# Performance work log

Hardware: AMD Instinct MI355X
Metric: run time of the kernel (lower is better)

The kernel has to match this reference:

```python
import jax, jax.numpy as jnp
import numpy as np

T, R, H, DK = 2, 3, 4, 32
IN_DIM, OUT_DIM = 128, 128
N = 50000
E = 400000
RELS = [(0, 1), (1, 0), (1, 1)]  # (src_type, dst_type) per relation


def setup_inputs() -> dict:
    key = jax.random.key(0)
    ks = jax.random.split(key, 24)
    lin_scale = float(np.sqrt(2.0 / (IN_DIM + OUT_DIM)))
    att_scale = float(np.sqrt(2.0 / (DK + DK)))
    inp = {
        'h0': jax.random.normal(ks[0], (N, IN_DIM), jnp.float32),
        'h1': jax.random.normal(ks[1], (N, IN_DIM), jnp.float32),
        'Wk': jax.random.normal(ks[2], (T, IN_DIM, OUT_DIM), jnp.float32) * lin_scale,
        'bk': jnp.zeros((T, OUT_DIM), jnp.float32),
        'Wq': jax.random.normal(ks[3], (T, IN_DIM, OUT_DIM), jnp.float32) * lin_scale,
        'bq': jnp.zeros((T, OUT_DIM), jnp.float32),
        'Wv': jax.random.normal(ks[4], (T, IN_DIM, OUT_DIM), jnp.float32) * lin_scale,
        'bv': jnp.zeros((T, OUT_DIM), jnp.float32),
        'Wa': jax.random.normal(ks[5], (T, OUT_DIM, OUT_DIM), jnp.float32) * lin_scale,
        'ba': jnp.zeros((T, OUT_DIM), jnp.float32),
        'rel_att': jax.random.normal(ks[6], (R, H, DK, DK), jnp.float32) * att_scale,
        'rel_msg': jax.random.normal(ks[7], (R, H, DK, DK), jnp.float32) * att_scale,
        'rel_pri': jnp.ones((R, H), jnp.float32),
        'skip': jnp.ones((T,), jnp.float32),
        'src0': jax.random.randint(ks[8], (E,), 0, N, jnp.int32),
        'dst0': jax.random.randint(ks[9], (E,), 0, N, jnp.int32),
        'src1': jax.random.randint(ks[10], (E,), 0, N, jnp.int32),
        'dst1': jax.random.randint(ks[11], (E,), 0, N, jnp.int32),
        'src2': jax.random.randint(ks[12], (E,), 0, N, jnp.int32),
        'dst2': jax.random.randint(ks[13], (E,), 0, N, jnp.int32),
    }
    return inp


def _hgt_forward(h0, h1, Wk, bk, Wq, bq, Wv, bv, Wa, ba,
                 rel_att, rel_msg, rel_pri, skip, edges):
    sqrt_dk = np.sqrt(DK).astype(np.float32)
    hs = [h0, h1]
    # per-type k/q/v projections, reshaped to [N, H, DK]
    k_all = [(hs[t] @ Wk[t] + bk[t]).reshape(-1, H, DK) for t in range(T)]
    q_all = [(hs[t] @ Wq[t] + bq[t]).reshape(-1, H, DK) for t in range(T)]
    v_all = [(hs[t] @ Wv[t] + bv[t]).reshape(-1, H, DK) for t in range(T)]
    agg = {0: [], 1: []}
    for r, (s, d) in enumerate(RELS):
        src, dst = edges[r]
        k = jnp.einsum('nhi,hij->nhj', k_all[s], rel_att[r])
        v = jnp.einsum('nhi,hij->nhj', v_all[s], rel_msg[r])
        q = q_all[d]
        # edge-wise dot-product attention score [E, H]
        score = jnp.einsum('ehd,ehd->eh', q[dst], k[src]) * rel_pri[r] / sqrt_dk
        # edge softmax normalized by destination node
        m = jax.ops.segment_max(score, dst, num_segments=N)
        e = jnp.exp(score - m[dst])
        z = jax.ops.segment_sum(e, dst, num_segments=N)
        a = e / z[dst]
        msg = v[src] * a[..., None]  # [E, H, DK]
        agg[d].append(jax.ops.segment_sum(msg, dst, num_segments=N))
    outs = []
    for t in range(T):
        tmean = agg[t][0]
        for extra in agg[t][1:]:
            tmean = tmean + extra
        tmean = tmean / jnp.float32(len(agg[t]))  # cross_reducer='mean'
        tt = tmean.reshape(-1, OUT_DIM)
        trans = tt @ Wa[t] + ba[t]  # dropout p=0 -> identity
        alpha = jax.nn.sigmoid(skip[t])
        outs.append(trans * alpha + hs[t] * (1.0 - alpha))
    return jnp.stack(outs)  # [T, N, OUT_DIM]


def reference(h0, h1, Wk, bk, Wq, bq, Wv, bv, Wa, ba,
              rel_att, rel_msg, rel_pri, skip,
              src0, dst0, src1, dst1, src2, dst2):
    edges = [(src0, dst0), (src1, dst1), (src2, dst2)]
    return _hgt_forward(h0, h1, Wk, bk, Wq, bq, Wv, bv, Wa, ba,
                        rel_att, rel_msg, rel_pri, skip, edges)
```

## Files before the change

kernel.cpp:

```cpp
#include <hip/hip_runtime.h>
#include <hip/hip_bf16.h>
#include <math.h>


#define NN 50000
#define EE 400000
#define CAP 40

typedef __bf16 bf16x8 __attribute__((ext_vector_type(8)));
typedef float floatx4 __attribute__((ext_vector_type(4)));
typedef _Float16 h2 __attribute__((ext_vector_type(2)));

#if __has_builtin(__builtin_amdgcn_exp2f)
#define EXP2F(x) __builtin_amdgcn_exp2f(x)
#else
#define EXP2F(x) exp2f(x)
#endif

__device__ __forceinline__ h2 u_to_h2(unsigned int u) {
    union { unsigned int u; h2 h; } x; x.u = u; return x.h;
}

__device__ __forceinline__ float dot2f(h2 a, h2 b, float c) {
#if __has_builtin(__builtin_amdgcn_fdot2)
    return __builtin_amdgcn_fdot2(a, b, c, false);
#else
    return fmaf((float)a.x, (float)b.x, fmaf((float)a.y, (float)b.y, c));
#endif
}

__device__ __forceinline__ float xor1_add(float x) {
#if __has_builtin(__builtin_amdgcn_mov_dpp)
    int y = __builtin_amdgcn_mov_dpp(__float_as_int(x), 0xB1, 0xf, 0xf, true);
    return x + __int_as_float(y);
#else
    return x + __shfl_xor(x, 1);
#endif
}
__device__ __forceinline__ float xor2_add(float x) {
#if __has_builtin(__builtin_amdgcn_mov_dpp)
    int y = __builtin_amdgcn_mov_dpp(__float_as_int(x), 0x4E, 0xf, 0xf, true);
    return x + __int_as_float(y);
#else
    return x + __shfl_xor(x, 2);
#endif
}
__device__ __forceinline__ float xor4_add(float x) {
#if __has_builtin(__builtin_amdgcn_ds_swizzle)
    int y = __builtin_amdgcn_ds_swizzle(__float_as_int(x), 0x101F);
    return x + __int_as_float(y);
#else
    return x + __shfl_xor(x, 4);
#endif
}

#define FUSEB 640
__global__ __launch_bounds__(256) void prep(
    const float* __restrict__ Wk, const float* __restrict__ bk,
    const float* __restrict__ Wq, const float* __restrict__ bq,
    const float* __restrict__ Wv, const float* __restrict__ bv,
    const float* __restrict__ rel_att, const float* __restrict__ rel_msg,
    const float* __restrict__ rel_pri, const float* __restrict__ Wa,
    __hip_bfloat16* __restrict__ Wcat0T, __hip_bfloat16* __restrict__ Wcat1T,
    __hip_bfloat16* __restrict__ WaT,
    float* __restrict__ bcat0, float* __restrict__ bcat1)
{
    int idx = blockIdx.x * 256 + threadIdx.x;
    const int R1 = 128 * 384, R2 = 128 * 640, R3 = 2 * 128 * 128;
    if (idx >= R1 + R2 + R3) return;
    if (idx >= R1 + R2) {
        int t = idx - R1 - R2;
        int tt = t >> 14, rem = t & 16383;
        int k = rem >> 7, col = rem & 127;
        WaT[tt * 16384 + col * 128 + k] = __float2bfloat16(Wa[tt * 16384 + k * 128 + col]);
        return;
    }
    int typ, i, col;
    __hip_bfloat16* Wout; float* bout;
    if (idx < R1) { typ = 0; i = idx / 384; col = idx % 384; Wout = Wcat0T; bout = bcat0; }
    else { idx -= R1; typ = 1; i = idx / 640; col = idx % 640; Wout = Wcat1T; bout = bcat1; }
    float w, b;
    if (col < 128) {
        w = Wq[(typ * 128 + i) * 128 + col];
        b = bq[typ * 128 + col];
    } else {
        int kvcol = col - 128;
        int r = (typ == 0) ? 0 : (1 + (kvcol >> 8));
        int gc = kvcol & 255;
        int isV = (gc >> 2) & 1;
        int c = (gc >> 3) * 4 + (gc & 3);
        int s = typ;
        const float* Wsrc = isV ? Wv : Wk;
        const float* bsrc = isV ? bv : bk;
        const float* rel  = isV ? rel_msg : rel_att;
        int h = c >> 5, j = c & 31;
        float acc = 0.f, bacc = 0.f;
        #pragma unroll
        for (int cc = 0; cc < 32; ++cc) {
            float rr = rel[((r * 4 + h) * 32 + cc) * 32 + j];
            acc  += Wsrc[(s * 128 + i) * 128 + h * 32 + cc] * rr;
            bacc += bsrc[s * 128 + h * 32 + cc] * rr;
        }
        if (!isV) {
            float sc = rel_pri[r * 4 + h] * (0.17677669529663687f * 1.4426950408889634f);
            acc *= sc; bacc *= sc;
        }
        w = acc; b = bacc;
    }
    Wout[col * 128 + i] = __float2bfloat16(w);
    if (i == 0) bout[col] = b;
}

#define SCATB 196
#define SCATX 294
__global__ __launch_bounds__(256) void proj_both(
    const float* __restrict__ h0, const float* __restrict__ h1,
    const __hip_bfloat16* __restrict__ W0T, const __hip_bfloat16* __restrict__ W1T,
    const float* __restrict__ b0, const float* __restrict__ b1,
    ushort* __restrict__ Q0, ushort* __restrict__ Q1,
    ushort* __restrict__ KV0, ushort* __restrict__ KV1,
    ushort* __restrict__ KV2,
    const int* __restrict__ s0, const int* __restrict__ d0,
    const int* __restrict__ s1, const int* __restrict__ d1,
    const int* __restrict__ s2, const int* __restrict__ d2,
    int* __restrict__ cursor, int* __restrict__ sorted_src)
{
    __shared__ __align__(16) __hip_bfloat16 As[128][136];
    __shared__ __align__(16) ushort Bs[128][136];
    const int tid = threadIdx.x;

    if (blockIdx.x < SCATX) {
        int sb = blockIdx.y * SCATX + blockIdx.x;
        int r = sb / SCATB;
        int blk = sb - r * SCATB;
        const int* S = (r == 0) ? s0 : (r == 1) ? s1 : s2;
        const int* D = (r == 0) ? d0 : (r == 1) ? d1 : d2;
        int e0 = blk * 2048 + tid * 8;
        if (e0 + 8 <= EE) {
            int sv[8], dv[8], pos[8];
            *(int4*)&sv[0] = *(const int4*)(S + e0);
            *(int4*)&sv[4] = *(const int4*)(S + e0 + 4);
            *(int4*)&dv[0] = *(const int4*)(D + e0);
            *(int4*)&dv[4] = *(const int4*)(D + e0 + 4);
            #pragma unroll
            for (int j = 0; j < 8; ++j)
                pos[j] = atomicAdd(&cursor[r * NN + dv[j]], 1);
            #pragma unroll
            for (int j = 0; j < 8; ++j)
                if (pos[j] < CAP)
                    sorted_src[(size_t)(r * NN + dv[j]) * CAP + pos[j]] = sv[j];
        } else {
            for (int j = 0; j < 8; ++j) {
                int e = e0 + j;
                if (e >= EE) break;
                int idx = r * NN + D[e];
                int pos = atomicAdd(&cursor[idx], 1);
                if (pos < CAP) sorted_src[(size_t)idx * CAP + pos] = S[e];
            }
        }
        return;
    }

    const int row0 = (blockIdx.x - SCATX) * 128;
    const int typ = blockIdx.y;
    const float* A = typ ? h1 : h0;
    const __hip_bfloat16* WT = typ ? W1T : W0T;
    const float* bias = typ ? b1 : b0;
    const int ntiles = typ ? 5 : 3;

    #pragma unroll
    for (int it = 0; it < 16; ++it) {
        int li = it * 256 + tid;
        int r = li >> 5, k4 = (li & 31) * 4;
        int grow = row0 + r;
        float4 a4 = make_float4(0.f, 0.f, 0.f, 0.f);
        if (grow < NN) a4 = *(const float4*)(A + (size_t)grow * 128 + k4);
        As[r][k4 + 0] = __float2bfloat16(a4.x);
        As[r][k4 + 1] = __float2bfloat16(a4.y);
        As[r][k4 + 2] = __float2bfloat16(a4.z);
        As[r][k4 + 3] = __float2bfloat16(a4.w);
    }

    const int lane = tid & 63;
    const int wv = tid >> 6;
    const int wr = (wv & 1) * 64, wc = (wv >> 1) * 64;
    const int lr = lane & 15, kq = lane >> 4;

    for (int ct = 0; ct < ntiles; ++ct) {
        __syncthreads();
        #pragma unroll
        for (int it = 0; it < 8; ++it) {
            int li = it * 256 + tid;
            int c = li >> 4, k8 = (li & 15) * 8;
            *(uint4*)&Bs[c][k8] = *(const uint4*)(WT + (size_t)(ct * 128 + c) * 128 + k8);
        }
        __syncthreads();

        floatx4 acc[4][4];
        #pragma unroll
        for (int i = 0; i < 4; ++i)
            #pragma unroll
            for (int j = 0; j < 4; ++j)
                acc[i][j] = (floatx4){0.f, 0.f, 0.f, 0.f};

        #pragma unroll
        for (int kc = 0; kc < 128; kc += 32) {
            bf16x8 a[4], b[4];
            #pragma unroll
            for (int i = 0; i < 4; ++i) a[i] = *(const bf16x8*)&As[wr + i * 16 + lr][kc + kq * 8];
            #pragma unroll
            for (int j = 0; j < 4; ++j) b[j] = *(const bf16x8*)&Bs[wc + j * 16 + lr][kc + kq * 8];
            #pragma unroll
            for (int i = 0; i < 4; ++i)
                #pragma unroll
                for (int j = 0; j < 4; ++j)
                    acc[i][j] = __builtin_amdgcn_mfma_f32_16x16x32_bf16(a[i], b[j], acc[i][j], 0, 0, 0);
        }

        float biasv[4];
        #pragma unroll
        for (int j = 0; j < 4; ++j) biasv[j] = bias[ct * 128 + wc + j * 16 + lr];

        __syncthreads();
        #pragma unroll
        for (int i = 0; i < 4; ++i)
            #pragma unroll
            for (int reg = 0; reg < 4; ++reg) {
                int row = wr + i * 16 + kq * 4 + reg;
                #pragma unroll
                for (int j = 0; j < 4; ++j) {
                    union { _Float16 h; ushort s; } cv;
                    cv.h = (_Float16)(acc[i][j][reg] + biasv[j]);
                    Bs[row][wc + j * 16 + lr] = cv.s;
                }
            }
        __syncthreads();

        ushort* plane; int ld, toff;
        if (ct == 0) { plane = typ ? Q1 : Q0; ld = 128; toff = 0; }
        else {
            int rel = typ ? (1 + ((ct - 1) >> 1)) : 0;
            plane = (rel == 0) ? KV0 : (rel == 1) ? KV1 : KV2;
            ld = 256; toff = ((ct - 1) & 1) * 128;
        }
        #pragma unroll
        for (int it = 0; it < 8; ++it) {
            int li = it * 256 + tid;
            int row = li >> 4, chunk = (li & 15) * 8;
            int grow = row0 + row;
            if (grow < NN)
                *(uint4*)(plane + (size_t)grow * ld + toff + chunk) = *(const uint4*)&Bs[row][chunk];
        }
    }
}

__device__ __forceinline__ void epi_body(
    char* smem,
    const __hip_bfloat16* __restrict__ A0, const __hip_bfloat16* __restrict__ A1, float ascale,
    const __hip_bfloat16* __restrict__ BT, const float* __restrict__ bias,
    float* __restrict__ C, const float* __restrict__ skipGate, const float* __restrict__ Hres)
{
    typedef __hip_bfloat16 bfrow[136];
    bfrow* As = (bfrow*)smem;
    bfrow* Bs = (bfrow*)(smem + 128 * 136 * 2);
    typedef float frow[132];
    frow* St = (frow*)smem;
    const int tid = threadIdx.x;
    const int row0 = blockIdx.x * 128;

    #pragma unroll
    for (int it = 0; it < 8; ++it) {
        int li = it * 256 + tid;
        int c = li >> 4, k8 = (li & 15) * 8;
        *(uint4*)&Bs[c][k8] = *(const uint4*)(BT + (size_t)c * 128 + k8);
    }
    #pragma unroll
    for (int it = 0; it < 8; ++it) {
        int li = it * 256 + tid;
        int r = li >> 4, k8 = (li & 15) * 8;
        int grow = row0 + r;
        __hip_bfloat162 o2[4];
        if (grow < NN) {
            const __hip_bfloat162* pa = (const __hip_bfloat162*)(A0 + (size_t)grow * 128 + k8);
            if (A1) {
                const __hip_bfloat162* pb = (const __hip_bfloat162*)(A1 + (size_t)grow * 128 + k8);
                #pragma unroll
                for (int u = 0; u < 4; ++u) {
                    float2 fa = __bfloat1622float2(pa[u]);
                    float2 fb = __bfloat1622float2(pb[u]);
                    fa.x = (fa.x + fb.x) * ascale;
                    fa.y = (fa.y + fb.y) * ascale;
                    o2[u] = __float22bfloat162_rn(fa);
                }
            } else {
                #pragma unroll
                for (int u = 0; u < 4; ++u) o2[u] = pa[u];
            }
        } else {
            __hip_bfloat162 zz = __float22bfloat162_rn(make_float2(0.f, 0.f));
            #pragma unroll
            for (int u = 0; u < 4; ++u) o2[u] = zz;
        }
        __hip_bfloat162* dst = (__hip_bfloat162*)&As[r][k8];
        #pragma unroll
        for (int u = 0; u < 4; ++u) dst[u] = o2[u];
    }
    __syncthreads();

    const int lane = tid & 63;
    const int wv = tid >> 6;
    const int wr = (wv & 1) * 64, wc = (wv >> 1) * 64;
    const int lr = lane & 15, kq = lane >> 4;

    floatx4 acc[4][4];
    #pragma unroll
    for (int i = 0; i < 4; ++i)
        #pragma unroll
        for (int j = 0; j < 4; ++j)
            acc[i][j] = (floatx4){0.f, 0.f, 0.f, 0.f};

    #pragma unroll
    for (int kc = 0; kc < 128; kc += 32) {
        bf16x8 a[4], b[4];
        #pragma unroll
        for (int i = 0; i < 4; ++i) a[i] = *(const bf16x8*)&As[wr + i * 16 + lr][kc + kq * 8];
        #pragma unroll
        for (int j = 0; j < 4; ++j) b[j] = *(const bf16x8*)&Bs[wc + j * 16 + lr][kc + kq * 8];
        #pragma unroll
        for (int i = 0; i < 4; ++i)
            #pragma unroll
            for (int j = 0; j < 4; ++j)
                acc[i][j] = __builtin_amdgcn_mfma_f32_16x16x32_bf16(a[i], b[j], acc[i][j], 0, 0, 0);
    }

    float sg = *skipGate;
    float alpha = 1.f / (1.f + expf(-sg));
    float beta = 1.f - alpha;
    float biasv[4];
    #pragma unroll
    for (int j = 0; j < 4; ++j) biasv[j] = bias[wc + j * 16 + lr];

    __syncthreads();
    #pragma unroll
    for (int i = 0; i < 4; ++i)
        #pragma unroll
        for (int reg = 0; reg < 4; ++reg) {
            int row = wr + i * 16 + kq * 4 + reg;
            #pragma unroll
            for (int j = 0; j < 4; ++j)
                St[row][wc + j * 16 + lr] = acc[i][j][reg] + biasv[j];
        }
    __syncthreads();

    #pragma unroll
    for (int it = 0; it < 16; ++it) {
        int li = it * 256 + tid;
        int row = li >> 5, chunk = (li & 31) * 4;
        int grow = row0 + row;
        if (grow < NN) {
            float4 v = *(const float4*)&St[row][chunk];
            float4 hr = *(const float4*)(Hres + (size_t)grow * 128 + chunk);
            v.x = v.x * alpha + hr.x * beta;
            v.y = v.y * alpha + hr.y * beta;
            v.z = v.z * alpha + hr.z * beta;
            v.w = v.w * alpha + hr.w * beta;
            *(float4*)(C + (size_t)grow * 128 + chunk) = v;
        }
    }
}

__global__ __launch_bounds__(256) void epi_both(
    const __hip_bfloat16* __restrict__ aggR0, const __hip_bfloat16* __restrict__ aggR1,
    const __hip_bfloat16* __restrict__ aggR2,
    const __hip_bfloat16* __restrict__ WaT, const float* __restrict__ ba,
    float* __restrict__ out, const float* __restrict__ skip,
    const float* __restrict__ h0, const float* __restrict__ h1)
{
    __shared__ __align__(16) char smem[128 * 136 * 2 * 2];
    if (blockIdx.y == 0)
        epi_body(smem, aggR1, nullptr, 1.f, WaT, ba, out, skip, h0);
    else
        epi_body(smem, aggR0, aggR2, 0.5f, WaT + 16384, ba + 128,
                 out + (size_t)NN * 128, skip + 1, h1);
}

__device__ __forceinline__ void edge4_accum(
    uint4 ra, uint4 rb, uint4 rc, uint4 rd,
    bool mA, bool mB, bool mC, bool mD,
    h2 q01, h2 q23,
    float& z, float& u0, float& u1, float& u2, float& u3)
{
    float pa = dot2f(u_to_h2(ra.x), q01, 0.f); pa = dot2f(u_to_h2(ra.y), q23, pa);
    float pb = dot2f(u_to_h2(rb.x), q01, 0.f); pb = dot2f(u_to_h2(rb.y), q23, pb);
    float pc = dot2f(u_to_h2(rc.x), q01, 0.f); pc = dot2f(u_to_h2(rc.y), q23, pc);
    float pd = dot2f(u_to_h2(rd.x), q01, 0.f); pd = dot2f(u_to_h2(rd.y), q23, pd);
    pa = xor1_add(pa); pb = xor1_add(pb); pc = xor1_add(pc); pd = xor1_add(pd);
    pa = xor2_add(pa); pb = xor2_add(pb); pc = xor2_add(pc); pd = xor2_add(pd);
    pa = xor4_add(pa); pb = xor4_add(pb); pc = xor4_add(pc); pd = xor4_add(pd);
    float ea = EXP2F(pa); if (!mA) ea = 0.f;
    float eb = EXP2F(pb); if (!mB) eb = 0.f;
    float ec = EXP2F(pc); if (!mC) ec = 0.f;
    float ed = EXP2F(pd); if (!mD) ed = 0.f;
    z += (ea + eb) + (ec + ed);
    h2 va, vb;
    va = u_to_h2(ra.z); vb = u_to_h2(ra.w);
    u0 = fmaf(ea, (float)va.x, u0); u1 = fmaf(ea, (float)va.y, u1);
    u2 = fmaf(ea, (float)vb.x, u2); u3 = fmaf(ea, (float)vb.y, u3);
    va = u_to_h2(rb.z); vb = u_to_h2(rb.w);
    u0 = fmaf(eb, (float)va.x, u0); u1 = fmaf(eb, (float)va.y, u1);
    u2 = fmaf(eb, (float)vb.x, u2); u3 = fmaf(eb, (float)vb.y, u3);
    va = u_to_h2(rc.z); vb = u_to_h2(rc.w);
    u0 = fmaf(ec, (float)va.x, u0); u1 = fmaf(ec, (float)va.y, u1);
    u2 = fmaf(ec, (float)vb.x, u2); u3 = fmaf(ec, (float)vb.y, u3);
    va = u_to_h2(rd.z); vb = u_to_h2(rd.w);
    u0 = fmaf(ed, (float)va.x, u0); u1 = fmaf(ed, (float)va.y, u1);
    u2 = fmaf(ed, (float)vb.x, u2); u3 = fmaf(ed, (float)vb.y, u3);
}

__global__ __launch_bounds__(256) void aggregate_all(
    const ushort* __restrict__ Q0, const ushort* __restrict__ Q1,
    const ushort* __restrict__ KV0, const ushort* __restrict__ KV1,
    const ushort* __restrict__ KV2,
    const int* __restrict__ sorted, const int* __restrict__ counts,
    __hip_bfloat16* __restrict__ aggR0, __hip_bfloat16* __restrict__ aggR1,
    __hip_bfloat16* __restrict__ aggR2)
{
    int n = (blockIdx.x * 256 + threadIdx.x) >> 6;
    int lane = threadIdx.x & 63;
    int r = blockIdx.y;
    const ushort *Q, *KV; __hip_bfloat16* outp;
    if (r == 0)      { Q = Q1; KV = KV0; outp = aggR0; }
    else if (r == 1) { Q = Q0; KV = KV1; outp = aggR1; }
    else             { Q = Q1; KV = KV2; outp = aggR2; }
    int gw = r * NN + n;

    int hl = lane & 31;
    int half = lane >> 5;

    int cnt = min(counts[gw], CAP);
    uint2 qr = *(const uint2*)(Q + (size_t)n * 128 + hl * 4);
    const int* elist = sorted + (size_t)gw * CAP;
    int4 v0 = *(const int4*)elist;
    int4 v1 = *(const int4*)(elist + 4);
    int4 v2 = *(const int4*)(elist + 8);
    int4 v3 = *(const int4*)(elist + 12);

    int i0 = half ? v0.y : v0.x;
    int i1 = half ? v0.w : v0.z;
    int i2 = half ? v1.y : v1.x;
    int i3 = half ? v1.w : v1.z;
    int j0 = half ? v2.y : v2.x;
    int j1 = half ? v2.w : v2.z;
    int j2 = half ? v3.y : v3.x;
    int j3 = half ? v3.w : v3.z;
    uint4 ra = *(const uint4*)(KV + (size_t)(unsigned)(i0 * 256 + hl * 8));
    uint4 rb = *(const uint4*)(KV + (size_t)(unsigned)(i1 * 256 + hl * 8));
    uint4 rc = *(const uint4*)(KV + (size_t)(unsigned)(i2 * 256 + hl * 8));
    uint4 rd = *(const uint4*)(KV + (size_t)(unsigned)(i3 * 256 + hl * 8));
    uint4 sa = *(const uint4*)(KV + (size_t)(unsigned)(j0 * 256 + hl * 8));
    uint4 sb = *(const uint4*)(KV + (size_t)(unsigned)(j1 * 256 + hl * 8));
    uint4 sc = *(const uint4*)(KV + (size_t)(unsigned)(j2 * 256 + hl * 8));
    uint4 sd = *(const uint4*)(KV + (size_t)(unsigned)(j3 * 256 + hl * 8));

    h2 q01 = u_to_h2(qr.x), q23 = u_to_h2(qr.y);

    bool mA = (0 + half) < cnt, mB = (2 + half) < cnt, mC = (4 + half) < cnt, mD = (6 + half) < cnt;
    float u0 = 0.f, u1 = 0.f, u2 = 0.f, u3 = 0.f, z = 0.f;
    edge4_accum(ra, rb, rc, rd, mA, mB, mC, mD, q01, q23, z, u0, u1, u2, u3);

    if (cnt > 8) {
        bool nA = (8 + half) < cnt, nB = (10 + half) < cnt, nC = (12 + half) < cnt, nD = (14 + half) < cnt;
        edge4_accum(sa, sb, sc, sd, nA, nB, nC, nD, q01, q23, z, u0, u1, u2, u3);

        for (int i = 16; i < cnt; i += 4) {
            int eA = i + half, eB = i + 2 + half;
            int sA = elist[min(eA, cnt - 1)];
            int sB = elist[min(eB, cnt - 1)];
            uint4 ta = *(const uint4*)(KV + (size_t)(unsigned)(sA * 256 + hl * 8));
            uint4 tb = *(const uint4*)(KV + (size_t)(unsigned)(sB * 256 + hl * 8));
            float pa = dot2f(u_to_h2(ta.x), q01, 0.f); pa = dot2f(u_to_h2(ta.y), q23, pa);
            float pb = dot2f(u_to_h2(tb.x), q01, 0.f); pb = dot2f(u_to_h2(tb.y), q23, pb);
            pa = xor1_add(pa); pb = xor1_add(pb);
            pa = xor2_add(pa); pb = xor2_add(pb);
            pa = xor4_add(pa); pb = xor4_add(pb);
            float ea = EXP2F(pa);
            float eb = EXP2F(pb);
            if (eA >= cnt) ea = 0.f;
            if (eB >= cnt) eb = 0.f;
            z += ea + eb;
            h2 va = u_to_h2(ta.z), vb = u_to_h2(ta.w);
            u0 = fmaf(ea, (float)va.x, u0); u1 = fmaf(ea, (float)va.y, u1);
            u2 = fmaf(ea, (float)vb.x, u2); u3 = fmaf(ea, (float)vb.y, u3);
            va = u_to_h2(tb.z); vb = u_to_h2(tb.w);
            u0 = fmaf(eb, (float)va.x, u0); u1 = fmaf(eb, (float)va.y, u1);
            u2 = fmaf(eb, (float)vb.x, u2); u3 = fmaf(eb, (float)vb.y, u3);
        }
    }

    z  += __shfl_xor(z, 32);
    u0 += __shfl_xor(u0, 32);
    u1 += __shfl_xor(u1, 32);
    u2 += __shfl_xor(u2, 32);
    u3 += __shfl_xor(u3, 32);
    if (half == 0) {
        float inv = (cnt > 0) ? 1.f / z : 0.f;
        __hip_bfloat162 o0 = __float22bfloat162_rn(make_float2(u0 * inv, u1 * inv));
        __hip_bfloat162 o1 = __float22bfloat162_rn(make_float2(u2 * inv, u3 * inv));
        union { uint2 u; __hip_bfloat162 h[2]; } pk2;
        pk2.h[0] = o0; pk2.h[1] = o1;
        *(uint2*)(outp + (size_t)n * 128 + hl * 4) = pk2.u;
    }
}

extern "C" void kernel_launch(void* const* d_in, const int* in_sizes, int n_in,
                              void* d_out, int out_size, void* d_ws, size_t ws_size,
                              hipStream_t stream)
{
    const float* h0      = (const float*)d_in[0];
    const float* h1      = (const float*)d_in[1];
    const float* Wk      = (const float*)d_in[2];
    const float* bk      = (const float*)d_in[3];
    const float* Wq      = (const float*)d_in[4];
    const float* bq      = (const float*)d_in[5];
    const float* Wv      = (const float*)d_in[6];
    const float* bv      = (const float*)d_in[7];
    const float* Wa      = (const float*)d_in[8];
    const float* ba      = (const float*)d_in[9];
    const float* rel_att = (const float*)d_in[10];
    const float* rel_msg = (const float*)d_in[11];
    const float* rel_pri = (const float*)d_in[12];
    const float* skip    = (const float*)d_in[13];
    const int*   src0    = (const int*)d_in[14];
    const int*   dst0    = (const int*)d_in[15];
    const int*   src1    = (const int*)d_in[16];
    const int*   dst1    = (const int*)d_in[17];
    const int*   src2    = (const int*)d_in[18];
    const int*   dst2    = (const int*)d_in[19];
    float* out = (float*)d_out;

    char* w = (char*)d_ws;
    auto alloc = [&](size_t bytes) -> char* {
        char* p = w; w += (bytes + 255) & ~(size_t)255; return p;
    };
    __hip_bfloat16* Wcat0T = (__hip_bfloat16*)alloc(384 * 128 * 2);
    __hip_bfloat16* Wcat1T = (__hip_bfloat16*)alloc(640 * 128 * 2);
    __hip_bfloat16* WaT    = (__hip_bfloat16*)alloc(2 * 128 * 128 * 2);
    float* bcat0 = (float*)alloc(384 * sizeof(float));
    float* bcat1 = (float*)alloc(640 * sizeof(float));
    ushort* Q0  = (ushort*)alloc((size_t)NN * 128 * 2);
    ushort* Q1  = (ushort*)alloc((size_t)NN * 128 * 2);
    ushort* KV0 = (ushort*)alloc((size_t)NN * 256 * 2);
    ushort* KV1 = (ushort*)alloc((size_t)NN * 256 * 2);
    ushort* KV2 = (ushort*)alloc((size_t)NN * 256 * 2);
    __hip_bfloat16* aggR0 = (__hip_bfloat16*)alloc((size_t)NN * 128 * 2);
    __hip_bfloat16* aggR1 = (__hip_bfloat16*)alloc((size_t)NN * 128 * 2);
    __hip_bfloat16* aggR2 = (__hip_bfloat16*)alloc((size_t)NN * 128 * 2);
    int* cursor  = (int*)alloc(3 * NN * sizeof(int));
    int* sorted  = (int*)alloc((size_t)3 * NN * CAP * sizeof(int));

    if ((size_t)(w - (char*)d_ws) > ws_size) return;

    size_t zlen = (size_t)((char*)sorted - (char*)cursor) + (size_t)3 * NN * CAP * sizeof(int);
    hipMemsetAsync(cursor, 0, zlen, stream);

    prep<<<FUSEB, 256, 0, stream>>>(
        Wk, bk, Wq, bq, Wv, bv, rel_att, rel_msg, rel_pri, Wa,
        Wcat0T, Wcat1T, WaT, bcat0, bcat1);

    const int ROWB = (NN + 127) / 128;
    proj_both<<<dim3(SCATX + ROWB, 2), 256, 0, stream>>>(
        h0, h1, Wcat0T, Wcat1T, bcat0, bcat1,
        Q0, Q1, KV0, KV1, KV2,
        src0, dst0, src1, dst1, src2, dst2, cursor, sorted);

    const int AG = (NN * 64) / 256;
    aggregate_all<<<dim3(AG, 3), 256, 0, stream>>>(Q0, Q1, KV0, KV1, KV2, sorted, cursor,
                                                   aggR0, aggR1, aggR2);

    epi_both<<<dim3(ROWB, 2), 256, 0, stream>>>(aggR0, aggR1, aggR2, WaT, ba, out, skip, h0, h1);
}
```

Measured before the change: 349.8 us.

## Replace global-atomic CSR build with two-pass shared-memory bucket sort

Edge bucketing by destination now runs as a two-pass bucket sort. The prep kernel partitions each edge block into 256-node destination buckets using shared-memory atomics, packing the source index and the low destination bits into one int. proj_both then gathers each bucket's slices, builds per-row lists in shared memory and writes them out coalesced, which removes the global atomics and the large workspace memset. It also defers the second group of KV loads in aggregation until cnt>8 and reuses the aggR0 buffer as scratch. The risks are silent truncation if a bucket slice overflows SLICE=40 and the 16-bit source packing, which only works because N fits in 16 bits.

```diff
diff --git a/kernel.cpp b/kernel.cpp
--- a/kernel.cpp
+++ b/kernel.cpp
@@ -6,6 +6,8 @@
 #define NN 50000
 #define EE 400000
 #define CAP 40
+#define NBKT 196
+#define SLICE 40
 
 typedef __bf16 bf16x8 __attribute__((ext_vector_type(8)));
 typedef float floatx4 __attribute__((ext_vector_type(4)));
@@ -63,8 +65,53 @@
     const float* __restrict__ rel_pri, const float* __restrict__ Wa,
     __hip_bfloat16* __restrict__ Wcat0T, __hip_bfloat16* __restrict__ Wcat1T,
     __hip_bfloat16* __restrict__ WaT,
-    float* __restrict__ bcat0, float* __restrict__ bcat1)
+    float* __restrict__ bcat0, float* __restrict__ bcat1,
+    const int* __restrict__ s0, const int* __restrict__ d0,
+    const int* __restrict__ s1, const int* __restrict__ d1,
+    const int* __restrict__ s2, const int* __restrict__ d2,
+    int* __restrict__ seg, int* __restrict__ cnt2)
 {
+    __shared__ int cur[NBKT];
+    if (blockIdx.x >= FUSEB) {
+        int ab = blockIdx.x - FUSEB;
+        int r = ab / NBKT;
+        int blk = ab - r * NBKT;
+        const int* S = (r == 0) ? s0 : (r == 1) ? s1 : s2;
+        const int* D = (r == 0) ? d0 : (r == 1) ? d1 : d2;
+        for (int t = threadIdx.x; t < NBKT; t += 256) cur[t] = 0;
+        __syncthreads();
+        int* segr = seg + (size_t)r * NBKT * NBKT * SLICE;
+        int e0 = blk * 2048 + threadIdx.x * 8;
+        if (e0 + 8 <= EE) {
+            int sv[8], dv[8];
+            *(int4*)&sv[0] = *(const int4*)(S + e0);
+            *(int4*)&sv[4] = *(const int4*)(S + e0 + 4);
+            *(int4*)&dv[0] = *(const int4*)(D + e0);
+            *(int4*)&dv[4] = *(const int4*)(D + e0 + 4);
+            #pragma unroll
+            for (int j = 0; j < 8; ++j) {
+                int d = dv[j];
+                int bkt = d >> 8;
+                int pos = atomicAdd(&cur[bkt], 1);
+                if (pos < SLICE)
+                    segr[((size_t)bkt * NBKT + blk) * SLICE + pos] = sv[j] | ((d & 255) << 16);
+            }
+        } else {
+            for (int j = 0; j < 8; ++j) {
+                int e = e0 + j;
+                if (e >= EE) break;
+                int d = D[e];
+                int bkt = d >> 8;
+                int pos = atomicAdd(&cur[bkt], 1);
+                if (pos < SLICE)
+                    segr[((size_t)bkt * NBKT + blk) * SLICE + pos] = S[e] | ((d & 255) << 16);
+            }
+        }
+        __syncthreads();
+        for (int t = threadIdx.x; t < NBKT; t += 256)
+            cnt2[((size_t)r * NBKT + blk) * NBKT + t] = min(cur[t], SLICE);
+        return;
+    }
     int idx = blockIdx.x * 256 + threadIdx.x;
     const int R1 = 128 * 384, R2 = 128 * 640, R3 = 2 * 128 * 128;
     if (idx >= R1 + R2 + R3) return;
@@ -111,7 +158,6 @@
     if (i == 0) bout[col] = b;
 }
 
-#define SCATB 196
 #define SCATX 294
 __global__ __launch_bounds__(256) void proj_both(
     const float* __restrict__ h0, const float* __restrict__ h1,
@@ -120,46 +166,61 @@
     ushort* __restrict__ Q0, ushort* __restrict__ Q1,
     ushort* __restrict__ KV0, ushort* __restrict__ KV1,
     ushort* __restrict__ KV2,
-    const int* __restrict__ s0, const int* __restrict__ d0,
-    const int* __restrict__ s1, const int* __restrict__ d1,
-    const int* __restrict__ s2, const int* __restrict__ d2,
-    int* __restrict__ cursor, int* __restrict__ sorted_src)
+    const int* __restrict__ seg, const int* __restrict__ cnt2,
+    int* __restrict__ sorted_src, int* __restrict__ counts)
 {
-    __shared__ __align__(16) __hip_bfloat16 As[128][136];
-    __shared__ __align__(16) ushort Bs[128][136];
+    __shared__ __align__(16) char smem[2 * 128 * 136 * 2];
     const int tid = threadIdx.x;
 
     if (blockIdx.x < SCATX) {
-        int sb = blockIdx.y * SCATX + blockIdx.x;
-        int r = sb / SCATB;
-        int blk = sb - r * SCATB;
-        const int* S = (r == 0) ? s0 : (r == 1) ? s1 : s2;
-        const int* D = (r == 0) ? d0 : (r == 1) ? d1 : d2;
-        int e0 = blk * 2048 + tid * 8;
-        if (e0 + 8 <= EE) {
-            int sv[8], dv[8], pos[8];
-            *(int4*)&sv[0] = *(const int4*)(S + e0);
-            *(int4*)&sv[4] = *(const int4*)(S + e0 + 4);
-            *(int4*)&dv[0] = *(const int4*)(D + e0);
-            *(int4*)&dv[4] = *(const int4*)(D + e0 + 4);
-            #pragma unroll
-            for (int j = 0; j < 8; ++j)
-                pos[j] = atomicAdd(&cursor[r * NN + dv[j]], 1);
-            #pragma unroll
-            for (int j = 0; j < 8; ++j)
-                if (pos[j] < CAP)
-                    sorted_src[(size_t)(r * NN + dv[j]) * CAP + pos[j]] = sv[j];
-        } else {
-            for (int j = 0; j < 8; ++j) {
-                int e = e0 + j;
-                if (e >= EE) break;
-                int idx = r * NN + D[e];
-                int pos = atomicAdd(&cursor[idx], 1);
-                if (pos < CAP) sorted_src[(size_t)idx * CAP + pos] = S[e];
+        int pb = blockIdx.y * SCATX + blockIdx.x;
+        int r = pb / NBKT;
+        int b = pb - r * NBKT;
+        int* stage  = (int*)smem;
+        int* cntl   = stage + 256 * CAP;
+        int* rowcnt = cntl + NBKT;
+        if (tid < NBKT) cntl[tid] = cnt2[((size_t)r * NBKT + tid) * NBKT + b];
+        rowcnt[tid] = 0;
+        int4 z4 = make_int4(0, 0, 0, 0);
+        #pragma unroll
+        for (int it = 0; it < (256 * CAP) / 4 / 256; ++it)
+            ((int4*)stage)[it * 256 + tid] = z4;
+        __syncthreads();
+
+        const int* segb = seg + (size_t)(r * NBKT + b) * (NBKT * SLICE);
+        const int NE4 = (NBKT * SLICE) / 4;
+        for (int li4 = tid; li4 < NE4; li4 += 256) {
+            int4 pv = ((const int4*)segb)[li4];
+            int pvals[4] = { pv.x, pv.y, pv.z, pv.w };
+            #pragma unroll
+            for (int j = 0; j < 4; ++j) {
+                int e = li4 * 4 + j;
+                int s = e / SLICE;
+                int k = e - s * SLICE;
+                if (k < cntl[s]) {
+                    int p = pvals[j];
+                    int dlow = (unsigned)p >> 16;
+                    int srcv = p & 0xFFFF;
+                    int pos = atomicAdd(&rowcnt[dlow], 1);
+                    if (pos < CAP) stage[dlow * CAP + pos] = srcv;
+                }
             }
         }
+        __syncthreads();
+
+        int nrows = min(256, NN - b * 256);
+        int* gout = sorted_src + ((size_t)r * NN + b * 256) * CAP;
+        int n4 = nrows * (CAP / 4);
+        for (int li = tid; li < n4; li += 256)
+            ((int4*)gout)[li] = ((int4*)stage)[li];
+        if (tid < nrows) counts[(size_t)r * NN + b * 256 + tid] = rowcnt[tid];
         return;
     }
+
+    typedef __hip_bfloat16 bfrow[136];
+    typedef ushort usrow[136];
+    bfrow* As = (bfrow*)smem;
+    usrow* Bs = (usrow*)(smem + 128 * 136 * 2);
 
     const int row0 = (blockIdx.x - SCATX) * 128;
     const int typ = blockIdx.y;
@@ -457,10 +518,6 @@
     uint4 rb = *(const uint4*)(KV + (size_t)(unsigned)(i1 * 256 + hl * 8));
     uint4 rc = *(const uint4*)(KV + (size_t)(unsigned)(i2 * 256 + hl * 8));
     uint4 rd = *(const uint4*)(KV + (size_t)(unsigned)(i3 * 256 + hl * 8));
-    uint4 sa = *(const uint4*)(KV + (size_t)(unsigned)(j0 * 256 + hl * 8));
-    uint4 sb = *(const uint4*)(KV + (size_t)(unsigned)(j1 * 256 + hl * 8));
-    uint4 sc = *(const uint4*)(KV + (size_t)(unsigned)(j2 * 256 + hl * 8));
-    uint4 sd = *(const uint4*)(KV + (size_t)(unsigned)(j3 * 256 + hl * 8));
 
     h2 q01 = u_to_h2(qr.x), q23 = u_to_h2(qr.y);
 
@@ -469,6 +526,10 @@
     edge4_accum(ra, rb, rc, rd, mA, mB, mC, mD, q01, q23, z, u0, u1, u2, u3);
 
     if (cnt > 8) {
+        uint4 sa = *(const uint4*)(KV + (size_t)(unsigned)(j0 * 256 + hl * 8));
+        uint4 sb = *(const uint4*)(KV + (size_t)(unsigned)(j1 * 256 + hl * 8));
+        uint4 sc = *(const uint4*)(KV + (size_t)(unsigned)(j2 * 256 + hl * 8));
+        uint4 sd = *(const uint4*)(KV + (size_t)(unsigned)(j3 * 256 + hl * 8));
         bool nA = (8 + half) < cnt, nB = (10 + half) < cnt, nC = (12 + half) < cnt, nD = (14 + half) < cnt;
         edge4_accum(sa, sb, sc, sd, nA, nB, nC, nD, q01, q23, z, u0, u1, u2, u3);
 
@@ -555,26 +616,27 @@
     __hip_bfloat16* aggR0 = (__hip_bfloat16*)alloc((size_t)NN * 128 * 2);
     __hip_bfloat16* aggR1 = (__hip_bfloat16*)alloc((size_t)NN * 128 * 2);
     __hip_bfloat16* aggR2 = (__hip_bfloat16*)alloc((size_t)NN * 128 * 2);
-    int* cursor  = (int*)alloc(3 * NN * sizeof(int));
+    int* counts  = (int*)alloc(3 * NN * sizeof(int));
     int* sorted  = (int*)alloc((size_t)3 * NN * CAP * sizeof(int));
 
+    int* seg  = (int*)aggR0;
+    int* cnt2 = seg + (size_t)3 * NBKT * NBKT * SLICE;
+
     if ((size_t)(w - (char*)d_ws) > ws_size) return;
 
-    size_t zlen = (size_t)((char*)sorted - (char*)cursor) + (size_t)3 * NN * CAP * sizeof(int);
-    hipMemsetAsync(cursor, 0, zlen, stream);
-
-    prep<<<FUSEB, 256, 0, stream>>>(
+    prep<<<FUSEB + 3 * NBKT, 256, 0, stream>>>(
         Wk, bk, Wq, bq, Wv, bv, rel_att, rel_msg, rel_pri, Wa,
-        Wcat0T, Wcat1T, WaT, bcat0, bcat1);
+        Wcat0T, Wcat1T, WaT, bcat0, bcat1,
+        src0, dst0, src1, dst1, src2, dst2, seg, cnt2);
 
     const int ROWB = (NN + 127) / 128;
     proj_both<<<dim3(SCATX + ROWB, 2), 256, 0, stream>>>(
         h0, h1, Wcat0T, Wcat1T, bcat0, bcat1,
         Q0, Q1, KV0, KV1, KV2,
-        src0, dst0, src1, dst1, src2, dst2, cursor, sorted);
+        seg, cnt2, sorted, counts);
 
     const int AG = (NN * 64) / 256;
-    aggregate_all<<<dim3(AG, 3), 256, 0, stream>>>(Q0, Q1, KV0, KV1, KV2, sorted, cursor,
+    aggregate_all<<<dim3(AG, 3), 256, 0, stream>>>(Q0, Q1, KV0, KV1, KV2, sorted, counts,
                                                    aggR0, aggR1, aggR2);
 
     epi_both<<<dim3(ROWB, 2), 256, 0, stream>>>(aggR0, aggR1, aggR2, WaT, ba, out, skip, h0, h1);
```

Measured after the change: 309.5 us. -11.5%, faster.
